# Optimization experiments

Hardware: AMD Instinct MI355X
Metric: run time of the kernel (lower is better)

Reference implementation:

```python
import jax, jax.numpy as jnp
import numpy as np
from jax.scipy.special import logsumexp

N, C = 8192, 4096
LOSS_WEIGHT = 1.0


def setup_inputs() -> dict:
    key = jax.random.key(0)
    k1, k2 = jax.random.split(key)
    cls_score = jax.random.normal(k1, (N, C), dtype=jnp.float32)
    label = jax.random.randint(k2, (N, C), 0, 2, dtype=jnp.int64)
    return {"cls_score": cls_score, "label": label}


def reference(cls_score, label):
    # pos/neg masks exactly as in the torch module
    pos = label >= 1
    neg = label == 0
    ninf = -jnp.inf
    # Torch builds an [N, C*C] tensor of (neg_k - pos_j) padded with a 0 column
    # and takes logsumexp over it. Algebraically:
    #   loss_i = logaddexp(0, logsumexp_k(pred[neg]) + logsumexp_j(-pred[pos]))
    lse_neg = logsumexp(jnp.where(neg, cls_score, ninf), axis=1)      # [N]
    lse_mpos = logsumexp(jnp.where(pos, -cls_score, ninf), axis=1)    # [N]
    loss = jnp.logaddexp(jnp.float32(0.0), lse_neg + lse_mpos)        # [N]
    # reduction='mean', loss_weight applied in forward
    return LOSS_WEIGHT * jnp.mean(loss)
```

## Files before the change

kernel.cpp:

```cpp
#include <hip/hip_runtime.h>
#include <hip/hip_bf16.h>

#define NROWS 8192
#define NCOLS 4096
#define NSC (NROWS * 4)
#define NBLK 2048
#define NWAVES (NBLK * 4)
#define ITERS (NSC / NWAVES)

typedef float v4f __attribute__((ext_vector_type(4)));
typedef int   v4i __attribute__((ext_vector_type(4)));
typedef float v2f __attribute__((ext_vector_type(2)));


__global__ __launch_bounds__(256) void partial_kernel(
        const float* __restrict__ score,
        const int* __restrict__ label,
        v2f* __restrict__ part) {
    const int w = blockIdx.x * 4 + (threadIdx.x >> 6);
    const int lane = threadIdx.x & 63;
    const v4f* __restrict__ s4 = reinterpret_cast<const v4f*>(score);
    const v4i* __restrict__ l4 = reinterpret_cast<const v4i*>(label);

#pragma unroll 1
    for (int it = 0; it < ITERS; ++it) {
        const int g = it * NWAVES + w;
        const size_t base = (size_t)g * 256 + lane;

        v4f fa[4]; v4i la[4];
#pragma unroll
        for (int j = 0; j < 4; ++j) {
            fa[j] = __builtin_nontemporal_load(&s4[base + j * 64]);
            la[j] = __builtin_nontemporal_load(&l4[base + j * 64]);
        }
        __builtin_amdgcn_sched_barrier(0);

        float sn = 0.0f, sp = 0.0f;
#pragma unroll
        for (int j = 0; j < 4; ++j) {
#pragma unroll
            for (int k = 0; k < 4; ++k) {
                float x = fa[j][k];
                bool neg = (la[j][k] == 0);
                float e = __expf(neg ? x : -x);
                sn += neg ? e : 0.0f;
                sp += neg ? 0.0f : e;
            }
        }
#pragma unroll
        for (int off = 32; off > 0; off >>= 1) {
            sn += __shfl_down(sn, off, 64);
            sp += __shfl_down(sp, off, 64);
        }
        if (lane == 0) {
            v2f r; r.x = sn; r.y = sp;
            __builtin_nontemporal_store(r, &part[g]);
        }
    }
}

__global__ __launch_bounds__(128) void row_reduce_kernel(
        const v2f* __restrict__ part,
        float* __restrict__ blocksum) {
    const int r = blockIdx.x * 128 + threadIdx.x;
    const v4f* __restrict__ p4 = reinterpret_cast<const v4f*>(part);
    v4f a = p4[2 * r], b = p4[2 * r + 1];
    float sn = (a[0] + a[2]) + (b[0] + b[2]);
    float sp = (a[1] + a[3]) + (b[1] + b[3]);
    float loss;
    if (sn <= 0.0f || sp <= 0.0f) {
        loss = 0.0f;
    } else {
        float z = logf(sn) + logf(sp);
        loss = fmaxf(z, 0.0f) + log1pf(__expf(-fabsf(z)));
    }
#pragma unroll
    for (int off = 32; off > 0; off >>= 1) loss += __shfl_down(loss, off, 64);
    __shared__ float ls[2];
    if ((threadIdx.x & 63) == 0) ls[threadIdx.x >> 6] = loss;
    __syncthreads();
    if (threadIdx.x == 0) blocksum[blockIdx.x] = ls[0] + ls[1];
}

__global__ __launch_bounds__(64) void final_kernel(
        const float* __restrict__ blocksum,
        float* __restrict__ out) {
    float s = blocksum[threadIdx.x];
#pragma unroll
    for (int off = 32; off > 0; off >>= 1) s += __shfl_down(s, off, 64);
    if (threadIdx.x == 0) out[0] = s * (1.0f / (float)NROWS);
}

extern "C" void kernel_launch(void* const* d_in, const int* in_sizes, int n_in,
                              void* d_out, int out_size, void* d_ws, size_t ws_size,
                              hipStream_t stream) {
    const float* score = (const float*)d_in[0];
    const int*   label = (const int*)d_in[1];
    v2f*   part     = (v2f*)d_ws;
    float* blocksum = (float*)((char*)d_ws + NSC * 8);
    float* out      = (float*)d_out;

    partial_kernel<<<NBLK, 256, 0, stream>>>(score, label, part);
    row_reduce_kernel<<<NROWS / 128, 128, 0, stream>>>(part, blocksum);
    final_kernel<<<1, 64, 0, stream>>>(blocksum, out);
}
```

Measured before the change: 252.1 us.

## Double-buffer tile loads in partial kernel and halve the grid

The partial kernel now uses two register buffers and issues the next tile's loads before reducing the current tile, so global-memory latency overlaps the exp/shuffle work. The grid drops from 2048 to 1024 blocks, giving each wave twice as many iterations, and launch bounds request 4 blocks per SIMD. This doubles per-thread register use for loaded data and lowers the number of waves in flight, which could cut the latency hiding that occupancy was providing.

```diff
diff --git a/kernel.cpp b/kernel.cpp
--- a/kernel.cpp
+++ b/kernel.cpp
@@ -4,7 +4,7 @@
 #define NROWS 8192
 #define NCOLS 4096
 #define NSC (NROWS * 4)
-#define NBLK 2048
+#define NBLK 1024
 #define NWAVES (NBLK * 4)
 #define ITERS (NSC / NWAVES)
 
@@ -13,7 +13,42 @@
 typedef float v2f __attribute__((ext_vector_type(2)));
 
 
-__global__ __launch_bounds__(256) void partial_kernel(
+#define LOAD_TILE(F, L, gg)                                                  \
+    do {                                                                     \
+        const size_t b_ = (size_t)(gg) * 256 + lane;                         \
+        _Pragma("unroll")                                                    \
+        for (int j_ = 0; j_ < 4; ++j_) {                                     \
+            F[j_] = __builtin_nontemporal_load(&s4[b_ + j_ * 64]);           \
+            L[j_] = __builtin_nontemporal_load(&l4[b_ + j_ * 64]);           \
+        }                                                                    \
+    } while (0)
+
+#define CONSUME_TILE(F, L, gg)                                               \
+    do {                                                                     \
+        float sn = 0.0f, sp = 0.0f;                                          \
+        _Pragma("unroll")                                                    \
+        for (int j_ = 0; j_ < 4; ++j_) {                                     \
+            _Pragma("unroll")                                                \
+            for (int k_ = 0; k_ < 4; ++k_) {                                 \
+                float x_ = F[j_][k_];                                        \
+                bool neg_ = (L[j_][k_] == 0);                                \
+                float e_ = __expf(neg_ ? x_ : -x_);                          \
+                sn += neg_ ? e_ : 0.0f;                                      \
+                sp += neg_ ? 0.0f : e_;                                      \
+            }                                                                \
+        }                                                                    \
+        _Pragma("unroll")                                                    \
+        for (int off_ = 32; off_ > 0; off_ >>= 1) {                          \
+            sn += __shfl_down(sn, off_, 64);                                 \
+            sp += __shfl_down(sp, off_, 64);                                 \
+        }                                                                    \
+        if (lane == 0) {                                                     \
+            v2f r_; r_.x = sn; r_.y = sp;                                    \
+            __builtin_nontemporal_store(r_, &part[gg]);                      \
+        }                                                                    \
+    } while (0)
+
+__global__ __launch_bounds__(256, 4) void partial_kernel(
         const float* __restrict__ score,
         const int* __restrict__ label,
         v2f* __restrict__ part) {
@@ -22,40 +57,24 @@
     const v4f* __restrict__ s4 = reinterpret_cast<const v4f*>(score);
     const v4i* __restrict__ l4 = reinterpret_cast<const v4i*>(label);
 
+    v4f fA[4], fB[4]; v4i lA[4], lB[4];
+
+    LOAD_TILE(fA, lA, w);
+    __builtin_amdgcn_sched_barrier(0);
+
 #pragma unroll 1
-    for (int it = 0; it < ITERS; ++it) {
-        const int g = it * NWAVES + w;
-        const size_t base = (size_t)g * 256 + lane;
-
-        v4f fa[4]; v4i la[4];
-#pragma unroll
-        for (int j = 0; j < 4; ++j) {
-            fa[j] = __builtin_nontemporal_load(&s4[base + j * 64]);
-            la[j] = __builtin_nontemporal_load(&l4[base + j * 64]);
-        }
+    for (int it = 0; it < ITERS; it += 2) {
+        const int gA = it * NWAVES + w;
+        const int gB = gA + NWAVES;
+        const int gA2 = gB + NWAVES;
+        if (it + 1 < ITERS) LOAD_TILE(fB, lB, gB);
         __builtin_amdgcn_sched_barrier(0);
-
-        float sn = 0.0f, sp = 0.0f;
-#pragma unroll
-        for (int j = 0; j < 4; ++j) {
-#pragma unroll
-            for (int k = 0; k < 4; ++k) {
-                float x = fa[j][k];
-                bool neg = (la[j][k] == 0);
-                float e = __expf(neg ? x : -x);
-                sn += neg ? e : 0.0f;
-                sp += neg ? 0.0f : e;
-            }
-        }
-#pragma unroll
-        for (int off = 32; off > 0; off >>= 1) {
-            sn += __shfl_down(sn, off, 64);
-            sp += __shfl_down(sp, off, 64);
-        }
-        if (lane == 0) {
-            v2f r; r.x = sn; r.y = sp;
-            __builtin_nontemporal_store(r, &part[g]);
-        }
+        CONSUME_TILE(fA, lA, gA);
+        __builtin_amdgcn_sched_barrier(0);
+        if (it + 2 < ITERS) LOAD_TILE(fA, lA, gA2);
+        __builtin_amdgcn_sched_barrier(0);
+        if (it + 1 < ITERS) CONSUME_TILE(fB, lB, gB);
+        __builtin_amdgcn_sched_barrier(0);
     }
 }
 
```

After: 251.3 us. About the same (-0.3%).
